# Performance work log

Measured on AMD Instinct MI355X. Metric: run time of the kernel, lower is better.

Reference implementation:

```python
import jax, jax.numpy as jnp
import numpy as np

EMBED = 1024
HEADS = 16
HEAD_DIM = EMBED // HEADS
B, L = 4, 2048


def setup_inputs() -> dict:
    key = jax.random.key(0)
    ks = jax.random.split(key, 10)
    s = 1.0 / np.sqrt(EMBED)
    x = jax.random.normal(ks[0], (B, L, EMBED), dtype=jnp.float32)
    mask = jax.random.randint(ks[1], (B, 1, L, L), 0, 2, dtype=jnp.int32)
    Wq = jax.random.normal(ks[2], (EMBED, EMBED), dtype=jnp.float32) * s
    Wk = jax.random.normal(ks[3], (EMBED, EMBED), dtype=jnp.float32) * s
    Wv = jax.random.normal(ks[4], (EMBED, EMBED), dtype=jnp.float32) * s
    Wo = jax.random.normal(ks[5], (EMBED, EMBED), dtype=jnp.float32) * s
    bq = jnp.zeros((EMBED,), jnp.float32)
    bk = jnp.zeros((EMBED,), jnp.float32)
    bv = jnp.zeros((EMBED,), jnp.float32)
    bo = jnp.zeros((EMBED,), jnp.float32)
    return {"x": x, "mask": mask, "Wq": Wq, "bq": bq, "Wk": Wk, "bk": bk,
            "Wv": Wv, "bv": bv, "Wo": Wo, "bo": bo}


def reference(x, mask, Wq, bq, Wk, bk, Wv, bv, Wo, bo):
    n, l, _ = x.shape
    q = (x @ Wq + bq).reshape(n, l, HEADS, HEAD_DIM)
    k = (x @ Wk + bk).reshape(n, l, HEADS, HEAD_DIM)
    v = (x @ Wv + bv).reshape(n, l, HEADS, HEAD_DIM)
    # [n, h, q, k] scores
    energy = jnp.einsum('nqhd,nkhd->nhqk', q, k)
    energy = jnp.where(mask == 0, jnp.float32(-1e20), energy)
    attn = jax.nn.softmax(energy / jnp.sqrt(jnp.float32(HEAD_DIM)), axis=-1)
    out = jnp.einsum('nhqk,nkhd->nqhd', attn, v).reshape(n, l, EMBED)
    return out @ Wo + bo
```

## Files before the change

### kernel.cpp

```cpp
#include <hip/hip_runtime.h>
#include <hip/hip_bf16.h>

#define EMBED 1024
#define HEADS 16
#define HDIM 64
#define BATCH 4
#define SEQ 2048
#define ROWS (BATCH * SEQ)
#define LOG2E 1.4426950408889634f

typedef __attribute__((ext_vector_type(8))) short bf16x8;
typedef __attribute__((ext_vector_type(4))) float f32x4;

#define MFMA16(a, b, c) __builtin_amdgcn_mfma_f32_16x16x32_bf16(a, b, c, 0, 0, 0)

__device__ __forceinline__ unsigned short f2bf(float f) {
    union { float f; unsigned int u; } x; x.f = f;
    unsigned int r = x.u + 0x7fffu + ((x.u >> 16) & 1u);
    return (unsigned short)(r >> 16);
}

__device__ __forceinline__ ushort2 pk2(float a, float b) {
    union { __hip_bfloat162 h; ushort2 u; } c;
    c.h = __float22bfloat162_rn(make_float2(a, b));
    return c.u;
}

__device__ __forceinline__ void gl2lds(const unsigned short* g, unsigned short* l) {
    __builtin_amdgcn_global_load_lds(
        (const __attribute__((address_space(1))) unsigned int*)g,
        (__attribute__((address_space(3))) unsigned int*)l, 16, 0, 0);
}

__global__ __launch_bounds__(256) void cvt_x_kernel(
    const float* __restrict__ in, unsigned short* __restrict__ out)
{
    int i = (blockIdx.x * 256 + threadIdx.x) * 4;
    float4 v = *(const float4*)(in + i);
    ushort2 a = pk2(v.x, v.y), b = pk2(v.z, v.w);
    ushort4 o; o.x = a.x; o.y = a.y; o.z = b.x; o.w = b.y;
    *(ushort4*)(out + i) = o;
}

__global__ __launch_bounds__(256) void wtrans_kernel(
    const float* __restrict__ W0, const float* __restrict__ W1,
    const float* __restrict__ W2, const float* __restrict__ W3,
    unsigned short* __restrict__ Wt)
{
    __shared__ float t[32][33];
    const float* W = (blockIdx.z == 0) ? W0 : (blockIdx.z == 1) ? W1
                   : (blockIdx.z == 2) ? W2 : W3;
    unsigned short* o = Wt + (size_t)blockIdx.z * EMBED * EMBED;
    int tx = threadIdx.x & 31, ty = threadIdx.x >> 5;
    int bx = blockIdx.x * 32, by = blockIdx.y * 32;
#pragma unroll
    for (int r = 0; r < 32; r += 8)
        t[ty + r][tx] = W[(size_t)(by + ty + r) * EMBED + bx + tx];
    __syncthreads();
#pragma unroll
    for (int r = 0; r < 32; r += 8)
        o[(size_t)(bx + ty + r) * EMBED + by + tx] = f2bf(t[tx][ty + r]);
}

__global__ __launch_bounds__(256) void cvt_mask_kernel(
    const int* __restrict__ in, unsigned char* __restrict__ out)
{
    int i = (blockIdx.x * 256 + threadIdx.x) * 4;
    int4 v = *(const int4*)(in + i);
    uchar4 o;
    o.x = v.x != 0; o.y = v.y != 0; o.z = v.z != 0; o.w = v.w != 0;
    *(uchar4*)(out + i) = o;
}

__global__ __launch_bounds__(256) void vtrans_kernel(
    const unsigned short* __restrict__ Vb, unsigned short* __restrict__ Vt)
{
    __shared__ unsigned short t[64][72];
    int b = blockIdx.z, h = blockIdx.y, k0 = blockIdx.x * 64;
    int r = threadIdx.x >> 2, c = (threadIdx.x & 3) * 16;
    const unsigned short* src = Vb + (size_t)(b * SEQ + k0 + r) * EMBED + h * HDIM + c;
    *(uint4*)&t[r][c]     = *(const uint4*)(src);
    *(uint4*)&t[r][c + 8] = *(const uint4*)(src + 8);
    __syncthreads();
    unsigned short* dst = Vt + (size_t)((b * HEADS + h) * HDIM + r) * SEQ + k0 + c;
    union { unsigned short u[8]; uint4 v; } p0, p1;
#pragma unroll
    for (int i = 0; i < 8; i++) p0.u[i] = t[c + i][r];
#pragma unroll
    for (int i = 0; i < 8; i++) p1.u[i] = t[c + 8 + i][r];
    *(uint4*)dst       = p0.v;
    *(uint4*)(dst + 8) = p1.v;
}

__device__ __forceinline__ void gemm_bf16_body(
    const unsigned short* __restrict__ A, const unsigned short* __restrict__ Bt,
    const float* __restrict__ bias,
    float* __restrict__ outF, unsigned short* __restrict__ outB, float scale)
{
    __shared__ unsigned short As[128][32];
    __shared__ unsigned short Bs[128][32];
    const int tid = threadIdx.x;
    const int lane = tid & 63, wid = tid >> 6;
    const int ln = lane & 15, lg = lane >> 4;
    const int wy = wid >> 1, wx = wid & 1;
    const int m0 = blockIdx.y * 128, n0 = blockIdx.x * 128;
    const int srow = tid >> 2;
    const int scol = (tid & 3) * 8;
    const unsigned short* Ap = A + (size_t)(m0 + srow) * EMBED + scol;
    const unsigned short* Bp = Bt + (size_t)(n0 + srow) * EMBED + scol;
    unsigned short* lA = &As[srow & ~15][0];
    unsigned short* lB = &Bs[srow & ~15][0];

    f32x4 acc[4][4];
#pragma unroll
    for (int i = 0; i < 4; i++)
#pragma unroll
        for (int j = 0; j < 4; j++) acc[i][j] = (f32x4){0.f, 0.f, 0.f, 0.f};

    for (int k0 = 0; k0 < EMBED; k0 += 32) {
        __syncthreads();
        gl2lds(Ap + k0, lA);
        gl2lds(Ap + (size_t)64 * EMBED + k0, lA + 64 * 32);
        gl2lds(Bp + k0, lB);
        gl2lds(Bp + (size_t)64 * EMBED + k0, lB + 64 * 32);
        __syncthreads();
        bf16x8 af[4], bfr[4];
#pragma unroll
        for (int mi = 0; mi < 4; mi++)
            af[mi] = *(const bf16x8*)&As[wy * 64 + mi * 16 + ln][lg * 8];
#pragma unroll
        for (int nj = 0; nj < 4; nj++)
            bfr[nj] = *(const bf16x8*)&Bs[wx * 64 + nj * 16 + ln][lg * 8];
#pragma unroll
        for (int mi = 0; mi < 4; mi++)
#pragma unroll
            for (int nj = 0; nj < 4; nj++)
                acc[mi][nj] = MFMA16(af[mi], bfr[nj], acc[mi][nj]);
    }

#pragma unroll
    for (int mi = 0; mi < 4; mi++) {
#pragma unroll
        for (int nj = 0; nj < 4; nj++) {
            int row = m0 + wy * 64 + mi * 16 + lg * 4;
            int col = n0 + wx * 64 + nj * 16 + ln;
            float bv = bias[col];
#pragma unroll
            for (int r = 0; r < 4; r++) {
                float v = (acc[mi][nj][r] + bv) * scale;
                if (outF) outF[(size_t)(row + r) * EMBED + col] = v;
                else      outB[(size_t)(row + r) * EMBED + col] = f2bf(v);
            }
        }
    }
}

__global__ __launch_bounds__(256) void qkv_gemm_kernel(
    const unsigned short* __restrict__ Xb, const unsigned short* __restrict__ Wt,
    const float* __restrict__ bq, const float* __restrict__ bk,
    const float* __restrict__ bv,
    unsigned short* __restrict__ Qb, unsigned short* __restrict__ Kb,
    unsigned short* __restrict__ Vb)
{
    int z = blockIdx.z;
    const unsigned short* Bt = Wt + (size_t)z * EMBED * EMBED;
    const float* bias = (z == 0) ? bq : (z == 1) ? bk : bv;
    unsigned short* out = (z == 0) ? Qb : (z == 1) ? Kb : Vb;
    float scale = (z == 0) ? 0.125f * LOG2E : 1.0f;
    gemm_bf16_body(Xb, Bt, bias, nullptr, out, scale);
}

__global__ __launch_bounds__(256) void out_gemm_kernel(
    const unsigned short* __restrict__ Ob, const unsigned short* __restrict__ Wto,
    const float* __restrict__ bo, float* __restrict__ out)
{
    gemm_bf16_body(Ob, Wto, bo, out, nullptr, 1.0f);
}

__global__ __launch_bounds__(256) void attn_mfma_kernel(
    const unsigned short* __restrict__ Qb, const unsigned short* __restrict__ Kb,
    const unsigned short* __restrict__ Vt, const unsigned char* __restrict__ mask8,
    unsigned short* __restrict__ Ob)
{
    __shared__ unsigned short Ks[64][64];
    __shared__ unsigned short Vs[64][64];
    __shared__ unsigned short Ps[4][32][64];
    const int tid = threadIdx.x;
    const int lane = tid & 63, wid = tid >> 6;
    const int ln = lane & 15, lg = lane >> 4;
    const int b = blockIdx.z, h = blockIdx.y;
    const int q0 = blockIdx.x * 128 + wid * 32;

    bf16x8 qf[2][2];
#pragma unroll
    for (int mi = 0; mi < 2; mi++)
#pragma unroll
        for (int ks = 0; ks < 2; ks++)
            qf[mi][ks] = *(const bf16x8*)(Qb +
                (size_t)(b * SEQ + q0 + mi * 16 + ln) * EMBED + h * HDIM + ks * 32 + lg * 8);

    f32x4 o[2][4];
#pragma unroll
    for (int mi = 0; mi < 2; mi++)
#pragma unroll
        for (int dj = 0; dj < 4; dj++) o[mi][dj] = (f32x4){0.f, 0.f, 0.f, 0.f};
    float lsum[2] = {0.f, 0.f};

    const int srow = tid >> 3;
    const int scol = (tid & 7) * 8;
    const unsigned short* Kp = Kb + (size_t)(b * SEQ + srow) * EMBED + h * HDIM + scol;
    const unsigned short* Vp = Vt + (size_t)((b * HEADS + h) * HDIM + srow) * SEQ + scol;
    unsigned short* lK = &Ks[srow & ~7][0];
    unsigned short* lV = &Vs[srow & ~7][0];

    const unsigned char* mq0 = mask8 + (size_t)b * SEQ * SEQ + (size_t)(q0 + ln) * SEQ;
    const unsigned char* mq1 = mq0 + (size_t)16 * SEQ;

    int pwr[4], prd[2];
#pragma unroll
    for (int nj = 0; nj < 4; nj++)
        pwr[nj] = (((2 * nj + (lg >> 1)) ^ (ln & 7)) << 3) + ((lg & 1) << 2);
#pragma unroll
    for (int ks = 0; ks < 2; ks++)
        prd[ks] = ((4 * ks + lg) ^ (ln & 7)) << 3;
    unsigned short* ps0 = &Ps[wid][ln][0];
    unsigned short* ps1 = &Ps[wid][16 + ln][0];

    for (int kt = 0; kt < SEQ; kt += 64) {
        __syncthreads();
        gl2lds(Kp + (size_t)kt * EMBED, lK);
        gl2lds(Kp + (size_t)(kt + 32) * EMBED, lK + 32 * 64);
        gl2lds(Vp + kt, lV);
        gl2lds(Vp + (size_t)32 * SEQ + kt, lV + 32 * 64);
        __syncthreads();

        uchar4 mv[2][4];
#pragma unroll
        for (int mi = 0; mi < 2; mi++) {
            const unsigned char* mq = (mi ? mq1 : mq0) + kt;
#pragma unroll
            for (int nj = 0; nj < 4; nj++)
                mv[mi][nj] = *(const uchar4*)(mq + nj * 16 + lg * 4);
        }

        f32x4 S[2][4];
#pragma unroll
        for (int nj = 0; nj < 4; nj++) {
            bf16x8 k0 = *(const bf16x8*)&Ks[nj * 16 + ln][lg * 8];
            bf16x8 k1 = *(const bf16x8*)&Ks[nj * 16 + ln][32 + lg * 8];
#pragma unroll
            for (int mi = 0; mi < 2; mi++) {
                f32x4 t = (f32x4){0.f, 0.f, 0.f, 0.f};
                t = MFMA16(k0, qf[mi][0], t);
                t = MFMA16(k1, qf[mi][1], t);
                S[mi][nj] = t;
            }
        }

#pragma unroll
        for (int mi = 0; mi < 2; mi++) {
            unsigned short* psb = mi ? ps1 : ps0;
            float rs = 0.f;
#pragma unroll
            for (int nj = 0; nj < 4; nj++) {
                uchar4 m = mv[mi][nj];
                float p0 = m.x ? __builtin_amdgcn_exp2f(S[mi][nj][0]) : 0.f;
                float p1 = m.y ? __builtin_amdgcn_exp2f(S[mi][nj][1]) : 0.f;
                float p2 = m.z ? __builtin_amdgcn_exp2f(S[mi][nj][2]) : 0.f;
                float p3 = m.w ? __builtin_amdgcn_exp2f(S[mi][nj][3]) : 0.f;
                rs += (p0 + p1) + (p2 + p3);
                ushort2 w0 = pk2(p0, p1), w1 = pk2(p2, p3);
                ushort4 pw; pw.x = w0.x; pw.y = w0.y; pw.z = w1.x; pw.w = w1.y;
                *(ushort4*)(psb + pwr[nj]) = pw;
            }
            lsum[mi] += rs;
        }

#pragma unroll
        for (int ks = 0; ks < 2; ks++) {
            bf16x8 p0 = *(const bf16x8*)(ps0 + prd[ks]);
            bf16x8 p1 = *(const bf16x8*)(ps1 + prd[ks]);
#pragma unroll
            for (int dj = 0; dj < 4; dj++) {
                bf16x8 vf = *(const bf16x8*)&Vs[dj * 16 + ln][ks * 32 + lg * 8];
                o[0][dj] = MFMA16(p0, vf, o[0][dj]);
                o[1][dj] = MFMA16(p1, vf, o[1][dj]);
            }
        }
    }

#pragma unroll
    for (int mi = 0; mi < 2; mi++) {
        float l = lsum[mi];
        l += __shfl_xor(l, 16);
        l += __shfl_xor(l, 32);
        float li = 1.0f / l;
        float l0 = __shfl(li, lg * 4 + 0);
        float l1 = __shfl(li, lg * 4 + 1);
        float l2 = __shfl(li, lg * 4 + 2);
        float l3 = __shfl(li, lg * 4 + 3);
#pragma unroll
        for (int dj = 0; dj < 4; dj++) {
            unsigned short* op = Ob + (size_t)(b * SEQ + q0 + mi * 16 + lg * 4) * EMBED
                                    + h * HDIM + dj * 16 + ln;
            ushort2 w0 = pk2(o[mi][dj][0] * l0, o[mi][dj][1] * l1);
            ushort2 w1 = pk2(o[mi][dj][2] * l2, o[mi][dj][3] * l3);
            op[0]         = w0.x;
            op[EMBED]     = w0.y;
            op[2 * EMBED] = w1.x;
            op[3 * EMBED] = w1.y;
        }
    }
}

extern "C" void kernel_launch(void* const* d_in, const int* in_sizes, int n_in,
                              void* d_out, int out_size, void* d_ws, size_t ws_size,
                              hipStream_t stream)
{
    const float* x  = (const float*)d_in[0];
    const int* mask = (const int*)d_in[1];
    const float* Wq = (const float*)d_in[2];
    const float* bq = (const float*)d_in[3];
    const float* Wk = (const float*)d_in[4];
    const float* bk = (const float*)d_in[5];
    const float* Wv = (const float*)d_in[6];
    const float* bv = (const float*)d_in[7];
    const float* Wo = (const float*)d_in[8];
    const float* bo = (const float*)d_in[9];
    float* outp = (float*)d_out;

    char* ws = (char*)d_ws;
    unsigned short* Wt = (unsigned short*)(ws);
    unsigned char*  m8 = (unsigned char*)(ws + ((size_t)8 << 20));
    unsigned short* Xb = (unsigned short*)(ws + ((size_t)24 << 20));
    unsigned short* Vt = Xb;
    unsigned short* Qb = (unsigned short*)(ws + ((size_t)40 << 20));
    unsigned short* Kb = (unsigned short*)(ws + ((size_t)56 << 20));
    unsigned short* Vb = (unsigned short*)(ws + ((size_t)72 << 20));
    unsigned short* Ob = Vb;

    cvt_x_kernel<<<ROWS * EMBED / 1024, 256, 0, stream>>>(x, Xb);
    wtrans_kernel<<<dim3(32, 32, 4), 256, 0, stream>>>(Wq, Wk, Wv, Wo, Wt);
    cvt_mask_kernel<<<(size_t)BATCH * SEQ * SEQ / 1024, 256, 0, stream>>>(mask, m8);
    qkv_gemm_kernel<<<dim3(EMBED / 128, ROWS / 128, 3), 256, 0, stream>>>(
        Xb, Wt, bq, bk, bv, Qb, Kb, Vb);
    vtrans_kernel<<<dim3(SEQ / 64, HEADS, BATCH), 256, 0, stream>>>(Vb, Vt);
    attn_mfma_kernel<<<dim3(SEQ / 128, HEADS, BATCH), 256, 0, stream>>>(
        Qb, Kb, Vt, m8, Ob);
    out_gemm_kernel<<<dim3(EMBED / 128, ROWS / 128), 256, 0, stream>>>(
        Ob, Wt + (size_t)3 * EMBED * EMBED, bo, outp);
}
```

Baseline: 429.1 us.

## Swizzle LDS tiles, compute softmax row sums via MFMA, prefetch mask early

Applies XOR swizzles to the global-to-LDS staging and fragment reads in both the projection GEMM and the attention K/V tiles to avoid LDS bank conflicts. The per-row softmax denominator is now accumulated with an extra MFMA against a ones vector, using the bf16-rounded probabilities, which removes the scalar adds and the cross-lane shuffles. Mask bytes for the next tile are loaded before the barrier to hide their latency. This costs two extra MFMAs per k-step and makes the denominator use bf16-rounded P rather than fp32 values.

```diff
diff --git a/kernel.cpp b/kernel.cpp
--- a/kernel.cpp
+++ b/kernel.cpp
@@ -105,11 +105,12 @@
     const int wy = wid >> 1, wx = wid & 1;
     const int m0 = blockIdx.y * 128, n0 = blockIdx.x * 128;
     const int srow = tid >> 2;
-    const int scol = (tid & 3) * 8;
+    const int scol = (((tid & 3) ^ ((tid >> 2) & 3) ^ ((tid >> 4) & 3)) << 3);
     const unsigned short* Ap = A + (size_t)(m0 + srow) * EMBED + scol;
     const unsigned short* Bp = Bt + (size_t)(n0 + srow) * EMBED + scol;
     unsigned short* lA = &As[srow & ~15][0];
     unsigned short* lB = &Bs[srow & ~15][0];
+    const int swg = ((lg ^ (ln & 3) ^ (ln >> 2)) << 3);
 
     f32x4 acc[4][4];
 #pragma unroll
@@ -127,10 +128,10 @@
         bf16x8 af[4], bfr[4];
 #pragma unroll
         for (int mi = 0; mi < 4; mi++)
-            af[mi] = *(const bf16x8*)&As[wy * 64 + mi * 16 + ln][lg * 8];
+            af[mi] = *(const bf16x8*)&As[wy * 64 + mi * 16 + ln][swg];
 #pragma unroll
         for (int nj = 0; nj < 4; nj++)
-            bfr[nj] = *(const bf16x8*)&Bs[wx * 64 + nj * 16 + ln][lg * 8];
+            bfr[nj] = *(const bf16x8*)&Bs[wx * 64 + nj * 16 + ln][swg];
 #pragma unroll
         for (int mi = 0; mi < 4; mi++)
 #pragma unroll
@@ -199,22 +200,28 @@
             qf[mi][ks] = *(const bf16x8*)(Qb +
                 (size_t)(b * SEQ + q0 + mi * 16 + ln) * EMBED + h * HDIM + ks * 32 + lg * 8);
 
+    bf16x8 ones;
+#pragma unroll
+    for (int i = 0; i < 8; i++) ones[i] = (short)0x3F80;
+
     f32x4 o[2][4];
 #pragma unroll
     for (int mi = 0; mi < 2; mi++)
 #pragma unroll
         for (int dj = 0; dj < 4; dj++) o[mi][dj] = (f32x4){0.f, 0.f, 0.f, 0.f};
-    float lsum[2] = {0.f, 0.f};
+    f32x4 lacc[2] = {(f32x4){0.f, 0.f, 0.f, 0.f}, (f32x4){0.f, 0.f, 0.f, 0.f}};
 
     const int srow = tid >> 3;
-    const int scol = (tid & 7) * 8;
-    const unsigned short* Kp = Kb + (size_t)(b * SEQ + srow) * EMBED + h * HDIM + scol;
-    const unsigned short* Vp = Vt + (size_t)((b * HEADS + h) * HDIM + srow) * SEQ + scol;
+    const int scolKV = (((tid & 7) ^ ((tid >> 3) & 7)) << 3);
+    const unsigned short* Kp = Kb + (size_t)(b * SEQ + srow) * EMBED + h * HDIM + scolKV;
+    const unsigned short* Vp = Vt + (size_t)((b * HEADS + h) * HDIM + srow) * SEQ + scolKV;
     unsigned short* lK = &Ks[srow & ~7][0];
     unsigned short* lV = &Vs[srow & ~7][0];
 
     const unsigned char* mq0 = mask8 + (size_t)b * SEQ * SEQ + (size_t)(q0 + ln) * SEQ;
     const unsigned char* mq1 = mq0 + (size_t)16 * SEQ;
+
+    const int swk = ((lg ^ (ln & 7)) << 3);
 
     int pwr[4], prd[2];
 #pragma unroll
@@ -227,6 +234,15 @@
     unsigned short* ps1 = &Ps[wid][16 + ln][0];
 
     for (int kt = 0; kt < SEQ; kt += 64) {
+        uchar4 mv[2][4];
+#pragma unroll
+        for (int mi = 0; mi < 2; mi++) {
+            const unsigned char* mq = (mi ? mq1 : mq0) + kt;
+#pragma unroll
+            for (int nj = 0; nj < 4; nj++)
+                mv[mi][nj] = *(const uchar4*)(mq + nj * 16 + lg * 4);
+        }
+
         __syncthreads();
         gl2lds(Kp + (size_t)kt * EMBED, lK);
         gl2lds(Kp + (size_t)(kt + 32) * EMBED, lK + 32 * 64);
@@ -234,20 +250,11 @@
         gl2lds(Vp + (size_t)32 * SEQ + kt, lV + 32 * 64);
         __syncthreads();
 
-        uchar4 mv[2][4];
-#pragma unroll
-        for (int mi = 0; mi < 2; mi++) {
-            const unsigned char* mq = (mi ? mq1 : mq0) + kt;
-#pragma unroll
-            for (int nj = 0; nj < 4; nj++)
-                mv[mi][nj] = *(const uchar4*)(mq + nj * 16 + lg * 4);
-        }
-
         f32x4 S[2][4];
 #pragma unroll
         for (int nj = 0; nj < 4; nj++) {
-            bf16x8 k0 = *(const bf16x8*)&Ks[nj * 16 + ln][lg * 8];
-            bf16x8 k1 = *(const bf16x8*)&Ks[nj * 16 + ln][32 + lg * 8];
+            bf16x8 k0 = *(const bf16x8*)&Ks[nj * 16 + ln][swk];
+            bf16x8 k1 = *(const bf16x8*)&Ks[nj * 16 + ln][swk ^ 32];
 #pragma unroll
             for (int mi = 0; mi < 2; mi++) {
                 f32x4 t = (f32x4){0.f, 0.f, 0.f, 0.f};
@@ -260,7 +267,6 @@
 #pragma unroll
         for (int mi = 0; mi < 2; mi++) {
             unsigned short* psb = mi ? ps1 : ps0;
-            float rs = 0.f;
 #pragma unroll
             for (int nj = 0; nj < 4; nj++) {
                 uchar4 m = mv[mi][nj];
@@ -268,21 +274,21 @@
                 float p1 = m.y ? __builtin_amdgcn_exp2f(S[mi][nj][1]) : 0.f;
                 float p2 = m.z ? __builtin_amdgcn_exp2f(S[mi][nj][2]) : 0.f;
                 float p3 = m.w ? __builtin_amdgcn_exp2f(S[mi][nj][3]) : 0.f;
-                rs += (p0 + p1) + (p2 + p3);
                 ushort2 w0 = pk2(p0, p1), w1 = pk2(p2, p3);
                 ushort4 pw; pw.x = w0.x; pw.y = w0.y; pw.z = w1.x; pw.w = w1.y;
                 *(ushort4*)(psb + pwr[nj]) = pw;
             }
-            lsum[mi] += rs;
         }
 
 #pragma unroll
         for (int ks = 0; ks < 2; ks++) {
             bf16x8 p0 = *(const bf16x8*)(ps0 + prd[ks]);
             bf16x8 p1 = *(const bf16x8*)(ps1 + prd[ks]);
+            lacc[0] = MFMA16(p0, ones, lacc[0]);
+            lacc[1] = MFMA16(p1, ones, lacc[1]);
 #pragma unroll
             for (int dj = 0; dj < 4; dj++) {
-                bf16x8 vf = *(const bf16x8*)&Vs[dj * 16 + ln][ks * 32 + lg * 8];
+                bf16x8 vf = *(const bf16x8*)&Vs[dj * 16 + ln][swk ^ (ks << 5)];
                 o[0][dj] = MFMA16(p0, vf, o[0][dj]);
                 o[1][dj] = MFMA16(p1, vf, o[1][dj]);
             }
@@ -291,14 +297,10 @@
 
 #pragma unroll
     for (int mi = 0; mi < 2; mi++) {
-        float l = lsum[mi];
-        l += __shfl_xor(l, 16);
-        l += __shfl_xor(l, 32);
-        float li = 1.0f / l;
-        float l0 = __shfl(li, lg * 4 + 0);
-        float l1 = __shfl(li, lg * 4 + 1);
-        float l2 = __shfl(li, lg * 4 + 2);
-        float l3 = __shfl(li, lg * 4 + 3);
+        float l0 = 1.0f / lacc[mi][0];
+        float l1 = 1.0f / lacc[mi][1];
+        float l2 = 1.0f / lacc[mi][2];
+        float l3 = 1.0f / lacc[mi][3];
 #pragma unroll
         for (int dj = 0; dj < 4; dj++) {
             unsigned short* op = Ob + (size_t)(b * SEQ + q0 + mi * 16 + lg * 4) * EMBED
```

Result: faster. 417.7 us (-2.7%).
